# Kernel optimization log

Measured on AMD Instinct MI355X. Metric: run time of the kernel, lower is better.

## Reference

```python
import jax, jax.numpy as jnp
import numpy as np

B, H = 1, 512
NVAR, NCLS = 16384, 65536
NP, NM = 4096, 4096
NEG = -1e30


def setup_inputs() -> dict:
    key = jax.random.key(0)
    ks = jax.random.split(key, 16)
    s = 0.02  # weight init scale
    return {
        "literal_emb": jax.random.normal(ks[0], (B, 2 * NVAR, H), jnp.float32),
        "clause_emb": jax.random.normal(ks[1], (B, NCLS, H), jnp.float32),
        "pos_idx": jax.random.randint(ks[2], (NP,), 0, NCLS),
        "neg_idx": jax.random.randint(ks[3], (NM,), 0, NCLS),
        "keep_mask": jax.random.randint(ks[4], (NP, NM), 0, 2).astype(bool),
        "taken_mask": jax.random.uniform(ks[5], (NP, NM)) < 0.01,  # sparse exclusion set
        "var_K_w": s * jax.random.normal(ks[6], (H, H), jnp.float32),
        "var_K_b": jnp.zeros((H,), jnp.float32),
        "var_Q_w": s * jax.random.normal(ks[7], (H, H), jnp.float32),
        "var_Q_b": jnp.zeros((H,), jnp.float32),
        "var_attn_w": s * jax.random.normal(ks[8], (1, H), jnp.float32),
        "var_attn_b": jnp.zeros((1,), jnp.float32),
        "W_Q_w": s * jax.random.normal(ks[9], (H, H), jnp.float32),
        "W_Q_b": jnp.zeros((H,), jnp.float32),
        "W_K_w": s * jax.random.normal(ks[10], (H, H), jnp.float32),
        "W_K_b": jnp.zeros((H,), jnp.float32),
    }


def reference(literal_emb, clause_emb, pos_idx, neg_idx, keep_mask, taken_mask,
              var_K_w, var_K_b, var_Q_w, var_Q_b, var_attn_w, var_attn_b,
              W_Q_w, W_Q_b, W_K_w, W_K_b):
    n_vars = literal_emb.shape[1] // 2
    # --- select_var: additive attention over positive literals ---
    K = literal_emb[:, :n_vars]                       # [B, V, H]
    K_t = K @ var_K_w.T + var_K_b                     # [B, V, H]
    Q = clause_emb.sum(axis=1)                        # [B, H] (C_aggr='sum')
    Q_t = Q @ var_Q_w.T + var_Q_b                     # [B, H]
    u = (jnp.tanh(K_t + Q_t[:, None, :]) @ var_attn_w.T + var_attn_b)[..., 0]  # [B, V]
    log_score = jax.nn.log_softmax(u, axis=-1)
    var_logp = jnp.max(log_score, axis=-1)            # [B]
    var_idx = jnp.argmax(log_score, axis=-1)          # [B]
    # --- clause-pair attention over pivot pos/neg clause pools ---
    q = clause_emb[:, pos_idx] @ W_Q_w.T + W_Q_b      # [B, NP, H]
    k = clause_emb[:, neg_idx] @ W_K_w.T + W_K_b      # [B, NM, H]
    h = q.shape[-1]
    scores = jnp.einsum('bnh,bmh->bnm', q, k) / jnp.sqrt(jnp.float32(h))
    # mask_grid_asym: drop invalid (keep_mask==0) and already-taken pairs, log-normalize
    valid = keep_mask & (~taken_mask)                 # [NP, NM]
    masked = jnp.where(valid[None], scores, jnp.float32(NEG))
    flat = masked.reshape(masked.shape[0], -1)        # [B, NP*NM]
    logp = jax.nn.log_softmax(flat, axis=-1)
    C_logp = jnp.max(logp, axis=-1)                   # [B]
    C_flat = jnp.argmax(logp, axis=-1)                # [B]
    M = scores.shape[-1]
    ci, cj = C_flat // M, C_flat % M
    c_idx_pos = pos_idx[ci]                           # map back to global clause ids
    c_idx_neg = neg_idx[cj]
    c_logp = C_logp + var_logp                        # [B]
    return (c_logp, c_idx_pos, c_idx_neg, var_idx)
```

## Files before the change

### kernel.cpp

```cpp
#include <hip/hip_runtime.h>
#include <hip/hip_bf16.h>
#include <math.h>

#define HH 512
#define NVARS 16384
#define NPOS 4096
#define NMS 4096
#define NEGV -1.0e30f
#define RSQRT_H 0.04419417382415922f

typedef unsigned short u16;
typedef __attribute__((ext_vector_type(8))) short bf16x8;
typedef __attribute__((ext_vector_type(4))) float f32x4;

struct SPart { float m; float s; int a; int pad; };

__device__ inline u16 f2bf(float f) {
  unsigned u = __float_as_uint(f);
  unsigned r = (u + 0x7fffu + ((u >> 16) & 1u)) >> 16;
  return (u16)r;
}
__device__ inline float bf2f(u16 h) { return __uint_as_float(((unsigned)h) << 16); }

__device__ inline void wreduce_maxidx(float& v, int& idx) {
#pragma unroll
  for (int m = 1; m < 64; m <<= 1) {
    float ov = __shfl_xor(v, m, 64);
    int oi = __shfl_xor(idx, m, 64);
    if (ov > v || (ov == v && oi < idx)) { v = ov; idx = oi; }
  }
}

__device__ inline float wreduce_sum(float v) {
#pragma unroll
  for (int m = 1; m < 64; m <<= 1) v += __shfl_xor(v, m, 64);
  return v;
}

__device__ __forceinline__ void stage_frag(const u16* src, u16* dst) {
  __builtin_amdgcn_global_load_lds(
      (const __attribute__((address_space(1))) void*)src,
      (__attribute__((address_space(3))) void*)dst, 16, 0, 0);
}

__device__ __forceinline__ void do_tofrag(
    const float* __restrict__ src, u16* __restrict__ hi, u16* __restrict__ lo,
    int frag, int lane) {
  const int R = frag >> 4, K = frag & 15;
  const float* p = src + (size_t)(R * 16 + (lane & 15)) * HH + K * 32 + (lane >> 4) * 8;
  float v[8];
  *(float4*)&v[0] = *(const float4*)p;
  *(float4*)&v[4] = *(const float4*)(p + 4);
  u16 h[8], l[8];
#pragma unroll
  for (int e = 0; e < 8; ++e) { h[e] = f2bf(v[e]); l[e] = f2bf(v[e] - bf2f(h[e])); }
  size_t base = (size_t)frag * 512 + (size_t)lane * 8;
  *(ushort4*)(hi + base) = *(ushort4*)&h[0];
  *(ushort4*)(hi + base + 4) = *(ushort4*)&h[4];
  *(ushort4*)(lo + base) = *(ushort4*)&l[0];
  *(ushort4*)(lo + base + 4) = *(ushort4*)&l[4];
}

__global__ __launch_bounds__(256) void wtofrag_kernel(
    const float* __restrict__ varKw, u16* __restrict__ wkhi, u16* __restrict__ wklo,
    const float* __restrict__ WQw, u16* __restrict__ pwqhi, u16* __restrict__ pwqlo,
    const float* __restrict__ WKw, u16* __restrict__ pwkhi, u16* __restrict__ pwklo) {
  const int wb = blockIdx.x;
  const int m = wb >> 7;
  const int frag = (wb & 127) * 4 + (threadIdx.x >> 6);
  const float* src = (m == 0) ? varKw : (m == 1) ? WQw : WKw;
  u16* hi = (m == 0) ? wkhi : (m == 1) ? pwqhi : pwkhi;
  u16* lo = (m == 0) ? wklo : (m == 1) ? pwqlo : pwklo;
  do_tofrag(src, hi, lo, frag, threadIdx.x & 63);
}

__global__ __launch_bounds__(256) void stream_kernel(
    const float* __restrict__ clause, double* __restrict__ qpart,
    const float* __restrict__ lit, u16* __restrict__ lithi, u16* __restrict__ litlo,
    const void* __restrict__ keep, const void* __restrict__ taken,
    unsigned long long* __restrict__ vmask) {
  const int bid = blockIdx.x;
  const int t = threadIdx.x;
  if (bid < 2048) {
    const int fg = t & 127;
    const int rh = t >> 7;
    const float* base = clause + ((size_t)bid * 32 + rh * 16) * HH + fg * 4;
    float4 v[16];
#pragma unroll
    for (int u = 0; u < 16; ++u)
      v[u] = *(const float4*)(base + (size_t)u * HH);
    double a0 = 0.0, a1 = 0.0, a2 = 0.0, a3 = 0.0;
#pragma unroll
    for (int u = 0; u < 16; ++u) {
      a0 += (double)v[u].x; a1 += (double)v[u].y;
      a2 += (double)v[u].z; a3 += (double)v[u].w;
    }
    double* o = qpart + (size_t)(bid * 2 + rh) * HH + fg * 4;
    o[0] = a0; o[1] = a1; o[2] = a2; o[3] = a3;
  } else if (bid < 6144) {
    const int frag = (bid - 2048) * 4 + (t >> 6);
    do_tofrag(lit, lithi, litlo, frag, t & 63);
  } else {
    __shared__ unsigned half_[256];
    const int pb = bid - 6144;
    const unsigned* kw = (const unsigned*)keep;
    int f = 1;
#pragma unroll
    for (int i = 0; i < 16; ++i) f &= (kw[i] <= 1u);
    const size_t e = (size_t)pb * 8192 + (size_t)t * 32;
    unsigned b = 0;
    if (f) {
      const unsigned* kp = (const unsigned*)keep + e;
      const unsigned* tp = (const unsigned*)taken + e;
      uint4 kv[8], tv[8];
#pragma unroll
      for (int c = 0; c < 8; ++c) { kv[c] = *(const uint4*)(kp + c * 4); }
#pragma unroll
      for (int c = 0; c < 8; ++c) { tv[c] = *(const uint4*)(tp + c * 4); }
#pragma unroll
      for (int c = 0; c < 8; ++c) {
        b |= (unsigned)(kv[c].x && !tv[c].x) << (c * 4 + 0);
        b |= (unsigned)(kv[c].y && !tv[c].y) << (c * 4 + 1);
        b |= (unsigned)(kv[c].z && !tv[c].z) << (c * 4 + 2);
        b |= (unsigned)(kv[c].w && !tv[c].w) << (c * 4 + 3);
      }
    } else {
      const unsigned char* kp = (const unsigned char*)keep + e;
      const unsigned char* tp = (const unsigned char*)taken + e;
      uint4 k0 = *(const uint4*)kp, k1 = *(const uint4*)(kp + 16);
      uint4 t0 = *(const uint4*)tp, t1 = *(const uint4*)(tp + 16);
      unsigned kws[8] = {k0.x, k0.y, k0.z, k0.w, k1.x, k1.y, k1.z, k1.w};
      unsigned tws[8] = {t0.x, t0.y, t0.z, t0.w, t1.x, t1.y, t1.z, t1.w};
#pragma unroll
      for (int c = 0; c < 8; ++c)
#pragma unroll
        for (int y = 0; y < 4; ++y) {
          unsigned kb = (kws[c] >> (8 * y)) & 0xffu;
          unsigned tb = (tws[c] >> (8 * y)) & 0xffu;
          b |= (unsigned)(kb && !tb) << (c * 4 + y);
        }
    }
    half_[t] = b;
    __syncthreads();
    if (t < 128) {
      unsigned long long m = (unsigned long long)half_[t * 2] |
                             ((unsigned long long)half_[t * 2 + 1] << 32);
      vmask[(size_t)pb * 128 + t] = m;
    }
  }
}

__global__ __launch_bounds__(256) void qred_kernel(
    const double* __restrict__ qpart, double* __restrict__ Qd) {
  __shared__ double red[256];
  const int t = threadIdx.x;
  const int h = blockIdx.x * 16 + (t & 15);
  const int chunk = t >> 4;
  double s = 0.0;
  for (int j0 = 0; j0 < 256; j0 += 8) {
    double v[8];
#pragma unroll
    for (int u = 0; u < 8; ++u)
      v[u] = qpart[(size_t)(chunk * 256 + j0 + u) * HH + h];
#pragma unroll
    for (int u = 0; u < 8; ++u) s += v[u];
  }
  red[t] = s;
  __syncthreads();
  for (int off = 8; off > 0; off >>= 1) {
    if (chunk < off) red[t] += red[t + off * 16];
    __syncthreads();
  }
  if (t < 16) Qd[blockIdx.x * 16 + t] = red[t];
}

__global__ __launch_bounds__(256) void prepmv_kernel(
    const double* __restrict__ Qd, const float* __restrict__ varQw,
    const float* __restrict__ varQb, const float* __restrict__ varKb,
    float* __restrict__ tvec) {
  __shared__ double red[256];
  const int t = threadIdx.x;
  const int h = blockIdx.x * 16 + (t & 15);
  const int chunk = t >> 4;
  const float* wrow = varQw + (size_t)h * HH + chunk * 32;
  const double* qd = Qd + chunk * 32;
  double s = 0.0;
  for (int j = 0; j < 32; ++j) s += qd[j] * (double)wrow[j];
  red[t] = s;
  __syncthreads();
  for (int off = 8; off > 0; off >>= 1) {
    if (chunk < off) red[t] += red[t + off * 16];
    __syncthreads();
  }
  if (t < 16) {
    int hh = blockIdx.x * 16 + t;
    tvec[hh] = (float)(red[t] + (double)varQb[hh] + (double)varKb[hh]);
  }
}

#define MFMA16(A, B)                                                                 \
  _Pragma("unroll") for (int i_ = 0; i_ < 4; ++i_)                                   \
  _Pragma("unroll") for (int j_ = 0; j_ < 4; ++j_)                                   \
    acc[i_][j_] = __builtin_amdgcn_mfma_f32_16x16x32_bf16(A[i_], B[j_], acc[i_][j_], 0, 0, 0);

#define MFMAS(AH, AL, BH, BL)                                                        \
  do { MFMA16(AH, BH) MFMA16(AH, BL) MFMA16(AL, BH) } while (0)

__global__ __launch_bounds__(256, 3) void proj_kernel(
    const float* __restrict__ clause,
    const int* __restrict__ pos_idx, const int* __restrict__ neg_idx,
    const u16* __restrict__ pwqhi, const u16* __restrict__ pwqlo,
    const u16* __restrict__ pwkhi, const u16* __restrict__ pwklo,
    const float* __restrict__ bQ, const float* __restrict__ bK,
    u16* __restrict__ qhi, u16* __restrict__ qlo,
    u16* __restrict__ khi, u16* __restrict__ klo) {
  const int* __restrict__ idx = blockIdx.z ? neg_idx : pos_idx;
  const u16* __restrict__ whp = blockIdx.z ? pwkhi : pwqhi;
  const u16* __restrict__ wlp = blockIdx.z ? pwklo : pwqlo;
  const float* __restrict__ bias = blockIdx.z ? bK : bQ;
  u16* __restrict__ ohi = blockIdx.z ? khi : qhi;
  u16* __restrict__ olo = blockIdx.z ? klo : qlo;

  const int t = threadIdx.x, lane = t & 63, wid = t >> 6;
  const int wn = wid & 1, wm = wid >> 1;
  const int row0 = blockIdx.x * 128;
  const int col0 = blockIdx.y * 128;

  const float* bptr[4];
#pragma unroll
  for (int j = 0; j < 4; ++j) {
    int g = idx[row0 + wn * 64 + j * 16 + (lane & 15)];
    bptr[j] = clause + (size_t)g * HH + (lane >> 4) * 8;
  }
  const size_t abase = (size_t)((col0 >> 4) + wm * 4) * 8192 + (size_t)lane * 8;

  f32x4 acc[4][4] = {};
#pragma unroll
  for (int s = 0; s < 16; ++s) {
    float rB[4][8];
    bf16x8 aH[4], aL[4], bH[4], bL[4];
#pragma unroll
    for (int f = 0; f < 4; ++f) {
      *(float4*)&rB[f][0] = *(const float4*)(bptr[f] + s * 32);
      *(float4*)&rB[f][4] = *(const float4*)(bptr[f] + s * 32 + 4);
      size_t oa = abase + (size_t)f * 8192 + (size_t)s * 512;
      aH[f] = *(const bf16x8*)(whp + oa);
      aL[f] = *(const bf16x8*)(wlp + oa);
    }
#pragma unroll
    for (int f = 0; f < 4; ++f)
#pragma unroll
      for (int e = 0; e < 8; ++e) {
        float v = rB[f][e];
        u16 h = f2bf(v);
        bH[f][e] = (short)h;
        bL[f][e] = (short)f2bf(v - bf2f(h));
      }
    MFMA16(aH, bH)
    MFMA16(aL, bH)
    MFMA16(aH, bL)
  }

  const int q4 = lane >> 4;
#pragma unroll
  for (int i = 0; i < 4; ++i) {
    const int hbase = col0 + wm * 64 + i * 16 + q4 * 4;
    float b0 = bias[hbase + 0], b1 = bias[hbase + 1];
    float b2 = bias[hbase + 2], b3 = bias[hbase + 3];
    const int lane16 = (lane & 15) + ((i & 1) * 2 + (q4 >> 1)) * 16;
    const int sub = (q4 & 1) * 4;
#pragma unroll
    for (int j = 0; j < 4; ++j) {
      const int frag = ((row0 + wn * 64 + j * 16) >> 4) * 16 +
                       ((col0 + wm * 64 + i * 16) >> 5);
      size_t base = (size_t)frag * 512 + (size_t)lane16 * 8 + sub;
      ushort4 hv, lv;
      float v;
      v = acc[i][j][0] + b0; hv.x = f2bf(v); lv.x = f2bf(v - bf2f(hv.x));
      v = acc[i][j][1] + b1; hv.y = f2bf(v); lv.y = f2bf(v - bf2f(hv.y));
      v = acc[i][j][2] + b2; hv.z = f2bf(v); lv.z = f2bf(v - bf2f(hv.z));
      v = acc[i][j][3] + b3; hv.w = f2bf(v); lv.w = f2bf(v - bf2f(hv.w));
      *(ushort4*)(ohi + base) = hv;
      *(ushort4*)(olo + base) = lv;
    }
  }
}

__global__ __launch_bounds__(256, 2) void ktu_kernel(
    const u16* __restrict__ lithi, const u16* __restrict__ litlo,
    const u16* __restrict__ wkhi, const u16* __restrict__ wklo,
    const float* __restrict__ tvec, const float* __restrict__ attnw,
    float* __restrict__ upart) {
  __shared__ __align__(16) u16 lds[2][4][8][512];
  const int t = threadIdx.x, lane = t & 63, wid = t >> 6;
  const int wn = wid & 1, wm = wid >> 1;
  const int row0 = blockIdx.x * 128;
  const int l8 = lane * 8;

  const u16* sa = (wid == 0) ? lithi : (wid == 1) ? litlo : (wid == 2) ? wkhi : wklo;
  const int rb = (wid < 2) ? (row0 >> 4) : (blockIdx.y * 8);
  const u16* sab = sa + (size_t)rb * 8192 + l8;

#define KSTAGE(buf, s)                                                        \
  _Pragma("unroll") for (int f_ = 0; f_ < 8; ++f_)                            \
    stage_frag(sab + (size_t)f_ * 8192 + (size_t)(s) * 512,                   \
               &lds[buf][wid][f_][0]);

  KSTAGE(0, 0)
  f32x4 acc[4][4] = {};
#pragma unroll
  for (int s = 0; s < 16; ++s) {
    __syncthreads();
    if (s < 15) { KSTAGE((s + 1) & 1, s + 1) }
    const int b = s & 1;
    bf16x8 aH[4], aL[4], bH[4], bL[4];
#pragma unroll
    for (int f = 0; f < 4; ++f) {
      aH[f] = *(const bf16x8*)&lds[b][0][wn * 4 + f][l8];
      aL[f] = *(const bf16x8*)&lds[b][1][wn * 4 + f][l8];
      bH[f] = *(const bf16x8*)&lds[b][2][wm * 4 + f][l8];
      bL[f] = *(const bf16x8*)&lds[b][3][wm * 4 + f][l8];
    }
    MFMAS(aH, aL, bH, bL);
  }
#undef KSTAGE

  const int cbase = blockIdx.y * 128 + wm * 64;
  float tv[4], aw[4];
#pragma unroll
  for (int j = 0; j < 4; ++j) {
    int c = cbase + j * 16 + (lane & 15);
    tv[j] = tvec[c]; aw[j] = attnw[c];
  }
  float us[4][4];
#pragma unroll
  for (int i = 0; i < 4; ++i)
#pragma unroll
    for (int r = 0; r < 4; ++r) {
      float s = 0.f;
#pragma unroll
      for (int j = 0; j < 4; ++j) {
        float x = acc[i][j][r] + tv[j];
        float th = 1.0f - 2.0f / (__expf(2.0f * x) + 1.0f);
        s += th * aw[j];
      }
      us[i][r] = s;
    }
#pragma unroll
  for (int m = 1; m < 16; m <<= 1)
#pragma unroll
    for (int i = 0; i < 4; ++i)
#pragma unroll
      for (int r = 0; r < 4; ++r) us[i][r] += __shfl_xor(us[i][r], m, 64);
  if ((lane & 15) == 0) {
#pragma unroll
    for (int i = 0; i < 4; ++i)
#pragma unroll
      for (int r = 0; r < 4; ++r) {
        int row = row0 + wn * 64 + i * 16 + (lane >> 4) * 4 + r;
        upart[(size_t)(blockIdx.y * 2 + wm) * NVARS + row] = us[i][r];
      }
  }
}

__global__ __launch_bounds__(256, 2) void scores_kernel(
    const u16* __restrict__ qhi, const u16* __restrict__ qlo,
    const u16* __restrict__ khi, const u16* __restrict__ klo,
    const unsigned long long* __restrict__ vmask, SPart* __restrict__ parts) {
  __shared__ __align__(16) u16 lds[2][4][8][512];
  __shared__ unsigned long long mrow[128][2];
  __shared__ float s_rv[4]; __shared__ int s_ri[4]; __shared__ float s_rs[4];
  __shared__ float s_bm; __shared__ int s_ba;

  const int t = threadIdx.x;
  const int lane = t & 63;
  const int wid = t >> 6;
  const int wn = wid & 1, wm = wid >> 1;
  const int l8 = lane * 8;

  const int bid = blockIdx.x;
  const int xcd = bid & 7, p = bid >> 3;
  const int sp = p >> 6, q = p & 63;
  const int g = xcd * 2 + sp;
  const int bx = (g & 3) * 8 + (q & 7);
  const int by = (g >> 2) * 8 + (q >> 3);

  const int n0 = by * 128;
  const int m0 = bx * 128;

  const u16* sa = (wid == 0) ? qhi : (wid == 1) ? qlo : (wid == 2) ? khi : klo;
  const int rb = (wid < 2) ? (n0 >> 4) : (m0 >> 4);
  const u16* sab = sa + (size_t)rb * 8192 + l8;

#define SSTAGE(buf, s)                                                        \
  _Pragma("unroll") for (int f_ = 0; f_ < 8; ++f_)                            \
    stage_frag(sab + (size_t)f_ * 8192 + (size_t)(s) * 512,                   \
               &lds[buf][wid][f_][0]);

  {
    int r = t >> 1, w = t & 1;
    mrow[r][w] = vmask[(size_t)(n0 + r) * (NMS / 64) + (m0 >> 6) + w];
  }

  SSTAGE(0, 0)
  f32x4 acc[4][4] = {};
#pragma unroll
  for (int s = 0; s < 16; ++s) {
    __syncthreads();
    if (s < 15) { SSTAGE((s + 1) & 1, s + 1) }
    const int b = s & 1;
    bf16x8 aH[4], aL[4], bH[4], bL[4];
#pragma unroll
    for (int f = 0; f < 4; ++f) {
      aH[f] = *(const bf16x8*)&lds[b][0][wn * 4 + f][l8];
      aL[f] = *(const bf16x8*)&lds[b][1][wn * 4 + f][l8];
      bH[f] = *(const bf16x8*)&lds[b][2][wm * 4 + f][l8];
      bL[f] = *(const bf16x8*)&lds[b][3][wm * 4 + f][l8];
    }
    MFMAS(aH, aL, bH, bL);
  }
#undef SSTAGE

  const int rbase = wn * 64 + (lane >> 4) * 4;
  const int cb15 = (lane & 15);

  float mv = NEGV; int mi = 0x7fffffff;
#pragma unroll
  for (int i = 0; i < 4; ++i) {
#pragma unroll
    for (int r = 0; r < 4; ++r) {
      int rl = rbase + i * 16 + r;
      unsigned long long ww = mrow[rl][wm];
      int gb = (n0 + rl) * NMS + m0;
#pragma unroll
      for (int j = 0; j < 4; ++j) {
        int bit = j * 16 + cb15;
        int cl = wm * 64 + bit;
        float sv = acc[i][j][r] * RSQRT_H;
        acc[i][j][r] = sv;
        bool valid = ((ww >> bit) & 1ull) != 0;
        if (valid && (sv > mv || (sv == mv && gb + cl < mi))) { mv = sv; mi = gb + cl; }
      }
    }
  }
  wreduce_maxidx(mv, mi);
  if ((t & 63) == 0) { s_rv[wid] = mv; s_ri[wid] = mi; }
  __syncthreads();
  if (t == 0) {
    float bm = s_rv[0]; int ba = s_ri[0];
    for (int w = 1; w < 4; ++w)
      if (s_rv[w] > bm || (s_rv[w] == bm && s_ri[w] < ba)) { bm = s_rv[w]; ba = s_ri[w]; }
    s_bm = bm; s_ba = ba;
  }
  __syncthreads();
  const float bm = s_bm;

  float se = 0.f;
#pragma unroll
  for (int i = 0; i < 4; ++i) {
#pragma unroll
    for (int r = 0; r < 4; ++r) {
      int rl = rbase + i * 16 + r;
      unsigned long long ww = mrow[rl][wm];
#pragma unroll
      for (int j = 0; j < 4; ++j) {
        int bit = j * 16 + cb15;
        bool valid = ((ww >> bit) & 1ull) != 0;
        if (valid) se += __expf(acc[i][j][r] - bm);
      }
    }
  }
  se = wreduce_sum(se);
  if ((t & 63) == 0) s_rs[wid] = se;
  __syncthreads();
  if (t == 0) {
    SPart pt;
    pt.m = s_bm;
    pt.s = s_rs[0] + s_rs[1] + s_rs[2] + s_rs[3];
    pt.a = s_ba; pt.pad = 0;
    parts[by * 32 + bx] = pt;
  }
}

__global__ __launch_bounds__(256) void usum_kernel(
    const float* __restrict__ upart, SPart* __restrict__ uparts2) {
  __shared__ float s_rv[4]; __shared__ int s_ri[4]; __shared__ float s_rs[4];
  __shared__ float s_bm; __shared__ int s_ba;
  const int t = threadIdx.x;
  const int i = blockIdx.x * 256 + t;
  float u = 0.f;
#pragma unroll
  for (int p = 0; p < 8; ++p) u += upart[(size_t)p * NVARS + i];
  float mv = u; int mi = i;
  wreduce_maxidx(mv, mi);
  if ((t & 63) == 0) { s_rv[t >> 6] = mv; s_ri[t >> 6] = mi; }
  __syncthreads();
  if (t == 0) {
    float bm = s_rv[0]; int ba = s_ri[0];
    for (int w = 1; w < 4; ++w)
      if (s_rv[w] > bm || (s_rv[w] == bm && s_ri[w] < ba)) { bm = s_rv[w]; ba = s_ri[w]; }
    s_bm = bm; s_ba = ba;
  }
  __syncthreads();
  float se = __expf(u - s_bm);
  se = wreduce_sum(se);
  if ((t & 63) == 0) s_rs[t >> 6] = se;
  __syncthreads();
  if (t == 0) {
    SPart p;
    p.m = s_bm;
    p.s = s_rs[0] + s_rs[1] + s_rs[2] + s_rs[3];
    p.a = s_ba; p.pad = 0;
    uparts2[blockIdx.x] = p;
  }
}

__global__ __launch_bounds__(256) void final_kernel(
    const SPart* __restrict__ uparts2, const SPart* __restrict__ parts,
    const int* __restrict__ pos_idx, const int* __restrict__ neg_idx,
    float* __restrict__ out) {
  __shared__ float s_rv[4]; __shared__ int s_ri[4]; __shared__ float s_rs[4];
  __shared__ float s_umax; __shared__ int s_uarg; __shared__ float s_usum;
  __shared__ float s_gm; __shared__ int s_ga;
  const int t = threadIdx.x;

  float mv = -3.0e38f; int mi = 0x7fffffff;
  SPart up;
  if (t < 64) {
    up = uparts2[t];
    mv = up.m; mi = up.a;
  }
  wreduce_maxidx(mv, mi);
  if ((t & 63) == 0) { s_rv[t >> 6] = mv; s_ri[t >> 6] = mi; }
  __syncthreads();
  if (t == 0) {
    float bm = s_rv[0]; int ba = s_ri[0];
    for (int w = 1; w < 4; ++w)
      if (s_rv[w] > bm || (s_rv[w] == bm && s_ri[w] < ba)) { bm = s_rv[w]; ba = s_ri[w]; }
    s_umax = bm; s_uarg = ba;
  }
  __syncthreads();
  float se = (t < 64) ? up.s * __expf(up.m - s_umax) : 0.f;
  se = wreduce_sum(se);
  if ((t & 63) == 0) s_rs[t >> 6] = se;
  __syncthreads();
  if (t == 0) s_usum = s_rs[0] + s_rs[1] + s_rs[2] + s_rs[3];
  __syncthreads();

  mv = NEGV; mi = 0x7fffffff;
  for (int i = t; i < 1024; i += 256) {
    SPart p = parts[i];
    if (p.m > mv || (p.m == mv && p.a < mi)) { mv = p.m; mi = p.a; }
  }
  wreduce_maxidx(mv, mi);
  if ((t & 63) == 0) { s_rv[t >> 6] = mv; s_ri[t >> 6] = mi; }
  __syncthreads();
  if (t == 0) {
    float bm = s_rv[0]; int ba = s_ri[0];
    for (int w = 1; w < 4; ++w)
      if (s_rv[w] > bm || (s_rv[w] == bm && s_ri[w] < ba)) { bm = s_rv[w]; ba = s_ri[w]; }
    s_gm = bm; s_ga = ba;
  }
  __syncthreads();
  const float gm = s_gm;
  float ss = 0.f;
  for (int i = t; i < 1024; i += 256) {
    SPart p = parts[i];
    ss += p.s * __expf(p.m - gm);
  }
  ss = wreduce_sum(ss);
  if ((t & 63) == 0) s_rs[t >> 6] = ss;
  __syncthreads();
  if (t == 0) {
    float gsum = s_rs[0] + s_rs[1] + s_rs[2] + s_rs[3];
    float c_logp = -logf(gsum) - logf(s_usum);
    int ga = s_ga;
    if (ga == 0x7fffffff) ga = 0;
    int ci = ga >> 12, cj = ga & 4095;
    out[0] = c_logp;
    out[1] = (float)pos_idx[ci];
    out[2] = (float)neg_idx[cj];
    out[3] = (float)s_uarg;
  }
}

extern "C" void kernel_launch(void* const* d_in, const int* in_sizes, int n_in,
                              void* d_out, int out_size, void* d_ws, size_t ws_size,
                              hipStream_t stream) {
  (void)in_sizes; (void)n_in; (void)out_size; (void)ws_size;
  const float* lit    = (const float*)d_in[0];
  const float* clause = (const float*)d_in[1];
  const int* pos_idx  = (const int*)d_in[2];
  const int* neg_idx  = (const int*)d_in[3];
  const void* keep    = d_in[4];
  const void* taken   = d_in[5];
  const float* varKw  = (const float*)d_in[6];
  const float* varKb  = (const float*)d_in[7];
  const float* varQw  = (const float*)d_in[8];
  const float* varQb  = (const float*)d_in[9];
  const float* attnw  = (const float*)d_in[10];
  const float* WQw    = (const float*)d_in[12];
  const float* WQb    = (const float*)d_in[13];
  const float* WKw    = (const float*)d_in[14];
  const float* WKb    = (const float*)d_in[15];

  char* ws = (char*)d_ws;
  size_t off = 0;
  auto alloc = [&](size_t b) {
    char* p = ws + off;
    off = (off + b + 255) & ~(size_t)255;
    return p;
  };
  double* qpart              = (double*)alloc((size_t)4096 * HH * 8);
  double* Qd                 = (double*)alloc(HH * 8);
  float* tvec                = (float*)alloc(HH * 4);
  float* upart               = (float*)alloc(8 * (size_t)NVARS * 4);
  unsigned long long* vmask  = (unsigned long long*)alloc((size_t)NPOS * (NMS / 64) * 8);
  u16* qhi                   = (u16*)alloc((size_t)NPOS * HH * 2);
  u16* qlo                   = (u16*)alloc((size_t)NPOS * HH * 2);
  u16* khi                   = (u16*)alloc((size_t)NMS * HH * 2);
  u16* klo                   = (u16*)alloc((size_t)NMS * HH * 2);
  u16* wkhi                  = (u16*)alloc((size_t)HH * HH * 2);
  u16* wklo                  = (u16*)alloc((size_t)HH * HH * 2);
  u16* pwqhi                 = (u16*)alloc((size_t)HH * HH * 2);
  u16* pwqlo                 = (u16*)alloc((size_t)HH * HH * 2);
  u16* pwkhi                 = (u16*)alloc((size_t)HH * HH * 2);
  u16* pwklo                 = (u16*)alloc((size_t)HH * HH * 2);
  u16* lithi                 = (u16*)alloc((size_t)NVARS * HH * 2);
  u16* litlo                 = (u16*)alloc((size_t)NVARS * HH * 2);
  SPart* parts               = (SPart*)alloc(1024 * sizeof(SPart));
  SPart* uparts2             = (SPart*)alloc(64 * sizeof(SPart));

  wtofrag_kernel<<<384, 256, 0, stream>>>(varKw, wkhi, wklo,
                                          WQw, pwqhi, pwqlo,
                                          WKw, pwkhi, pwklo);
  proj_kernel<<<dim3(32, 4, 2), 256, 0, stream>>>(clause, pos_idx, neg_idx,
                                                  pwqhi, pwqlo, pwkhi, pwklo,
                                                  WQb, WKb,
                                                  qhi, qlo, khi, klo);
  stream_kernel<<<8192, 256, 0, stream>>>(clause, qpart, lit, lithi, litlo,
                                          keep, taken, vmask);
  qred_kernel<<<32, 256, 0, stream>>>(qpart, Qd);
  prepmv_kernel<<<32, 256, 0, stream>>>(Qd, varQw, varQb, varKb, tvec);
  scores_kernel<<<1024, 256, 0, stream>>>(qhi, qlo, khi, klo, vmask, parts);
  ktu_kernel<<<dim3(128, 4), 256, 0, stream>>>(lithi, litlo, wkhi, wklo,
                                               tvec, attnw, upart);
  usum_kernel<<<64, 256, 0, stream>>>(upart, uparts2);
  final_kernel<<<1, 256, 0, stream>>>(uparts2, parts, pos_idx, neg_idx,
                                      (float*)d_out);
}
```

Measured before the change: 246.1 us.

## Fuse mask packing, clause sum and literal split into scores kernel

Merges the stream kernel and the scores kernel into one launch. The scores blocks now build their validity bitmask straight from keep/taken instead of going through a global vmask buffer. The other blocks of the same launch do the clause-sum partials and the literal hi/lo split. The scores GEMM also drops its double-buffered LDS staging and loads fragments straight from global memory into registers. This saves a launch and the vmask round trip and lets memory-bound work overlap MFMA work, at the cost of possibly worse load latency hiding and more register pressure.

```diff
diff --git a/kernel.cpp b/kernel.cpp
--- a/kernel.cpp
+++ b/kernel.cpp
@@ -10,6 +10,7 @@
 #define RSQRT_H 0.04419417382415922f
 
 typedef unsigned short u16;
+typedef unsigned char u8;
 typedef __attribute__((ext_vector_type(8))) short bf16x8;
 typedef __attribute__((ext_vector_type(4))) float f32x4;
 
@@ -60,6 +61,26 @@
   *(ushort4*)(lo + base) = *(ushort4*)&l[0];
   *(ushort4*)(lo + base + 4) = *(ushort4*)&l[4];
 }
+
+#define MFMA16(A, B)                                                                 \
+  _Pragma("unroll") for (int i_ = 0; i_ < 4; ++i_)                                   \
+  _Pragma("unroll") for (int j_ = 0; j_ < 4; ++j_)                                   \
+    acc[i_][j_] = __builtin_amdgcn_mfma_f32_16x16x32_bf16(A[i_], B[j_], acc[i_][j_], 0, 0, 0);
+
+#define MFMAS(AH, AL, BH, BL)                                                        \
+  do { MFMA16(AH, BH) MFMA16(AH, BL) MFMA16(AL, BH) } while (0)
+
+#define LOADF(s, AH, AL, BH, BL, PAH, PAL, PBH, PBL)                                 \
+  do {                                                                               \
+    _Pragma("unroll") for (int f_ = 0; f_ < 4; ++f_) {                               \
+      size_t oa_ = abase + (size_t)f_ * 8192 + (size_t)(s) * 512;                    \
+      size_t ob_ = bbase + (size_t)f_ * 8192 + (size_t)(s) * 512;                    \
+      AH[f_] = *(const bf16x8*)(PAH + oa_);                                          \
+      AL[f_] = *(const bf16x8*)(PAL + oa_);                                          \
+      BH[f_] = *(const bf16x8*)(PBH + ob_);                                          \
+      BL[f_] = *(const bf16x8*)(PBL + ob_);                                          \
+    }                                                                                \
+  } while (0)
 
 __global__ __launch_bounds__(256) void wtofrag_kernel(
     const float* __restrict__ varKw, u16* __restrict__ wkhi, u16* __restrict__ wklo,
@@ -73,138 +94,6 @@
   u16* lo = (m == 0) ? wklo : (m == 1) ? pwqlo : pwklo;
   do_tofrag(src, hi, lo, frag, threadIdx.x & 63);
 }
-
-__global__ __launch_bounds__(256) void stream_kernel(
-    const float* __restrict__ clause, double* __restrict__ qpart,
-    const float* __restrict__ lit, u16* __restrict__ lithi, u16* __restrict__ litlo,
-    const void* __restrict__ keep, const void* __restrict__ taken,
-    unsigned long long* __restrict__ vmask) {
-  const int bid = blockIdx.x;
-  const int t = threadIdx.x;
-  if (bid < 2048) {
-    const int fg = t & 127;
-    const int rh = t >> 7;
-    const float* base = clause + ((size_t)bid * 32 + rh * 16) * HH + fg * 4;
-    float4 v[16];
-#pragma unroll
-    for (int u = 0; u < 16; ++u)
-      v[u] = *(const float4*)(base + (size_t)u * HH);
-    double a0 = 0.0, a1 = 0.0, a2 = 0.0, a3 = 0.0;
-#pragma unroll
-    for (int u = 0; u < 16; ++u) {
-      a0 += (double)v[u].x; a1 += (double)v[u].y;
-      a2 += (double)v[u].z; a3 += (double)v[u].w;
-    }
-    double* o = qpart + (size_t)(bid * 2 + rh) * HH + fg * 4;
-    o[0] = a0; o[1] = a1; o[2] = a2; o[3] = a3;
-  } else if (bid < 6144) {
-    const int frag = (bid - 2048) * 4 + (t >> 6);
-    do_tofrag(lit, lithi, litlo, frag, t & 63);
-  } else {
-    __shared__ unsigned half_[256];
-    const int pb = bid - 6144;
-    const unsigned* kw = (const unsigned*)keep;
-    int f = 1;
-#pragma unroll
-    for (int i = 0; i < 16; ++i) f &= (kw[i] <= 1u);
-    const size_t e = (size_t)pb * 8192 + (size_t)t * 32;
-    unsigned b = 0;
-    if (f) {
-      const unsigned* kp = (const unsigned*)keep + e;
-      const unsigned* tp = (const unsigned*)taken + e;
-      uint4 kv[8], tv[8];
-#pragma unroll
-      for (int c = 0; c < 8; ++c) { kv[c] = *(const uint4*)(kp + c * 4); }
-#pragma unroll
-      for (int c = 0; c < 8; ++c) { tv[c] = *(const uint4*)(tp + c * 4); }
-#pragma unroll
-      for (int c = 0; c < 8; ++c) {
-        b |= (unsigned)(kv[c].x && !tv[c].x) << (c * 4 + 0);
-        b |= (unsigned)(kv[c].y && !tv[c].y) << (c * 4 + 1);
-        b |= (unsigned)(kv[c].z && !tv[c].z) << (c * 4 + 2);
-        b |= (unsigned)(kv[c].w && !tv[c].w) << (c * 4 + 3);
-      }
-    } else {
-      const unsigned char* kp = (const unsigned char*)keep + e;
-      const unsigned char* tp = (const unsigned char*)taken + e;
-      uint4 k0 = *(const uint4*)kp, k1 = *(const uint4*)(kp + 16);
-      uint4 t0 = *(const uint4*)tp, t1 = *(const uint4*)(tp + 16);
-      unsigned kws[8] = {k0.x, k0.y, k0.z, k0.w, k1.x, k1.y, k1.z, k1.w};
-      unsigned tws[8] = {t0.x, t0.y, t0.z, t0.w, t1.x, t1.y, t1.z, t1.w};
-#pragma unroll
-      for (int c = 0; c < 8; ++c)
-#pragma unroll
-        for (int y = 0; y < 4; ++y) {
-          unsigned kb = (kws[c] >> (8 * y)) & 0xffu;
-          unsigned tb = (tws[c] >> (8 * y)) & 0xffu;
-          b |= (unsigned)(kb && !tb) << (c * 4 + y);
-        }
-    }
-    half_[t] = b;
-    __syncthreads();
-    if (t < 128) {
-      unsigned long long m = (unsigned long long)half_[t * 2] |
-                             ((unsigned long long)half_[t * 2 + 1] << 32);
-      vmask[(size_t)pb * 128 + t] = m;
-    }
-  }
-}
-
-__global__ __launch_bounds__(256) void qred_kernel(
-    const double* __restrict__ qpart, double* __restrict__ Qd) {
-  __shared__ double red[256];
-  const int t = threadIdx.x;
-  const int h = blockIdx.x * 16 + (t & 15);
-  const int chunk = t >> 4;
-  double s = 0.0;
-  for (int j0 = 0; j0 < 256; j0 += 8) {
-    double v[8];
-#pragma unroll
-    for (int u = 0; u < 8; ++u)
-      v[u] = qpart[(size_t)(chunk * 256 + j0 + u) * HH + h];
-#pragma unroll
-    for (int u = 0; u < 8; ++u) s += v[u];
-  }
-  red[t] = s;
-  __syncthreads();
-  for (int off = 8; off > 0; off >>= 1) {
-    if (chunk < off) red[t] += red[t + off * 16];
-    __syncthreads();
-  }
-  if (t < 16) Qd[blockIdx.x * 16 + t] = red[t];
-}
-
-__global__ __launch_bounds__(256) void prepmv_kernel(
-    const double* __restrict__ Qd, const float* __restrict__ varQw,
-    const float* __restrict__ varQb, const float* __restrict__ varKb,
-    float* __restrict__ tvec) {
-  __shared__ double red[256];
-  const int t = threadIdx.x;
-  const int h = blockIdx.x * 16 + (t & 15);
-  const int chunk = t >> 4;
-  const float* wrow = varQw + (size_t)h * HH + chunk * 32;
-  const double* qd = Qd + chunk * 32;
-  double s = 0.0;
-  for (int j = 0; j < 32; ++j) s += qd[j] * (double)wrow[j];
-  red[t] = s;
-  __syncthreads();
-  for (int off = 8; off > 0; off >>= 1) {
-    if (chunk < off) red[t] += red[t + off * 16];
-    __syncthreads();
-  }
-  if (t < 16) {
-    int hh = blockIdx.x * 16 + t;
-    tvec[hh] = (float)(red[t] + (double)varQb[hh] + (double)varKb[hh]);
-  }
-}
-
-#define MFMA16(A, B)                                                                 \
-  _Pragma("unroll") for (int i_ = 0; i_ < 4; ++i_)                                   \
-  _Pragma("unroll") for (int j_ = 0; j_ < 4; ++j_)                                   \
-    acc[i_][j_] = __builtin_amdgcn_mfma_f32_16x16x32_bf16(A[i_], B[j_], acc[i_][j_], 0, 0, 0);
-
-#define MFMAS(AH, AL, BH, BL)                                                        \
-  do { MFMA16(AH, BH) MFMA16(AH, BL) MFMA16(AL, BH) } while (0)
 
 __global__ __launch_bounds__(256, 3) void proj_kernel(
     const float* __restrict__ clause,
@@ -286,6 +175,221 @@
   }
 }
 
+__global__ __launch_bounds__(256, 3) void mega_kernel(
+    const u16* __restrict__ qhi, const u16* __restrict__ qlo,
+    const u16* __restrict__ khi, const u16* __restrict__ klo,
+    const void* __restrict__ keep, const void* __restrict__ taken,
+    SPart* __restrict__ parts,
+    const float* __restrict__ clause, double* __restrict__ qpart,
+    const float* __restrict__ lit, u16* __restrict__ lithi, u16* __restrict__ litlo) {
+  __shared__ unsigned long long mrow[128][2];
+  __shared__ float s_rv[4]; __shared__ int s_ri[4]; __shared__ float s_rs[4];
+  __shared__ float s_bm; __shared__ int s_ba;
+
+  const int id = blockIdx.x;
+  const int t = threadIdx.x;
+  const int lane = t & 63;
+  const int wid = t >> 6;
+
+  if (id >= 3072) {
+    const int frag = (id - 3072) * 4 + wid;
+    do_tofrag(lit, lithi, litlo, frag, lane);
+    return;
+  }
+  if (id >= 1024) {
+    const int qb = id - 1024;
+    const int fg = t & 127;
+    const int rh = t >> 7;
+    const float* base = clause + ((size_t)qb * 32 + rh * 16) * HH + fg * 4;
+    float4 v[16];
+#pragma unroll
+    for (int u = 0; u < 16; ++u)
+      v[u] = *(const float4*)(base + (size_t)u * HH);
+    double a0 = 0.0, a1 = 0.0, a2 = 0.0, a3 = 0.0;
+#pragma unroll
+    for (int u = 0; u < 16; ++u) {
+      a0 += (double)v[u].x; a1 += (double)v[u].y;
+      a2 += (double)v[u].z; a3 += (double)v[u].w;
+    }
+    double* o = qpart + (size_t)(qb * 2 + rh) * HH + fg * 4;
+    o[0] = a0; o[1] = a1; o[2] = a2; o[3] = a3;
+    return;
+  }
+
+  const int wn = wid & 1, wm = wid >> 1;
+
+  const int bid = id;
+  const int xcd = bid & 7, p = bid >> 3;
+  const int sp = p >> 6, q = p & 63;
+  const int g = xcd * 2 + sp;
+  const int bx = (g & 3) * 8 + (q & 7);
+  const int by = (g >> 2) * 8 + (q >> 3);
+
+  const int n0 = by * 128;
+  const int m0 = bx * 128;
+
+  {
+    const int r = t >> 1, half = t & 1;
+    const unsigned* kw = (const unsigned*)keep;
+    int f = 1;
+#pragma unroll
+    for (int i = 0; i < 16; ++i) f &= (kw[i] <= 1u);
+    unsigned long long w = 0;
+    if (!f) {
+      const u8* kp = (const u8*)keep + (size_t)(n0 + r) * NMS + m0 + half * 64;
+      const u8* tp = (const u8*)taken + (size_t)(n0 + r) * NMS + m0 + half * 64;
+#pragma unroll
+      for (int c = 0; c < 4; ++c) {
+        uint4 kv = *(const uint4*)(kp + c * 16);
+        uint4 tv = *(const uint4*)(tp + c * 16);
+        unsigned kws[4] = {kv.x, kv.y, kv.z, kv.w};
+        unsigned tws[4] = {tv.x, tv.y, tv.z, tv.w};
+#pragma unroll
+        for (int wi = 0; wi < 4; ++wi)
+#pragma unroll
+          for (int y = 0; y < 4; ++y) {
+            unsigned kb = (kws[wi] >> (8 * y)) & 0xffu;
+            unsigned tb = (tws[wi] >> (8 * y)) & 0xffu;
+            w |= (unsigned long long)(kb && !tb) << (c * 16 + wi * 4 + y);
+          }
+      }
+    } else {
+      const unsigned* kp = (const unsigned*)keep + (size_t)(n0 + r) * NMS + m0 + half * 64;
+      const unsigned* tp = (const unsigned*)taken + (size_t)(n0 + r) * NMS + m0 + half * 64;
+#pragma unroll
+      for (int c = 0; c < 16; ++c) {
+        uint4 kv = *(const uint4*)(kp + c * 4);
+        uint4 tv = *(const uint4*)(tp + c * 4);
+        w |= (unsigned long long)(kv.x && !tv.x) << (c * 4 + 0);
+        w |= (unsigned long long)(kv.y && !tv.y) << (c * 4 + 1);
+        w |= (unsigned long long)(kv.z && !tv.z) << (c * 4 + 2);
+        w |= (unsigned long long)(kv.w && !tv.w) << (c * 4 + 3);
+      }
+    }
+    mrow[r][half] = w;
+  }
+
+  const size_t abase = (size_t)((n0 >> 4) + wn * 4) * 8192 + (size_t)lane * 8;
+  const size_t bbase = (size_t)((m0 >> 4) + wm * 4) * 8192 + (size_t)lane * 8;
+
+  f32x4 acc[4][4] = {};
+#pragma unroll
+  for (int s = 0; s < 16; ++s) {
+    bf16x8 aH[4], aL[4], bH[4], bL[4];
+    LOADF(s, aH, aL, bH, bL, qhi, qlo, khi, klo);
+    MFMAS(aH, aL, bH, bL);
+  }
+  __syncthreads();
+
+  const int rbase = wn * 64 + (lane >> 4) * 4;
+  const int cb15 = (lane & 15);
+
+  float mv = NEGV; int mi = 0x7fffffff;
+#pragma unroll
+  for (int i = 0; i < 4; ++i) {
+#pragma unroll
+    for (int r = 0; r < 4; ++r) {
+      int rl = rbase + i * 16 + r;
+      unsigned long long ww = mrow[rl][wm];
+      int gb = (n0 + rl) * NMS + m0;
+#pragma unroll
+      for (int j = 0; j < 4; ++j) {
+        int bit = j * 16 + cb15;
+        int cl = wm * 64 + bit;
+        float sv = acc[i][j][r] * RSQRT_H;
+        acc[i][j][r] = sv;
+        bool valid = ((ww >> bit) & 1ull) != 0;
+        if (valid && (sv > mv || (sv == mv && gb + cl < mi))) { mv = sv; mi = gb + cl; }
+      }
+    }
+  }
+  wreduce_maxidx(mv, mi);
+  if ((t & 63) == 0) { s_rv[wid] = mv; s_ri[wid] = mi; }
+  __syncthreads();
+  if (t == 0) {
+    float bm = s_rv[0]; int ba = s_ri[0];
+    for (int w = 1; w < 4; ++w)
+      if (s_rv[w] > bm || (s_rv[w] == bm && s_ri[w] < ba)) { bm = s_rv[w]; ba = s_ri[w]; }
+    s_bm = bm; s_ba = ba;
+  }
+  __syncthreads();
+  const float bm = s_bm;
+
+  float se = 0.f;
+#pragma unroll
+  for (int i = 0; i < 4; ++i) {
+#pragma unroll
+    for (int r = 0; r < 4; ++r) {
+      int rl = rbase + i * 16 + r;
+      unsigned long long ww = mrow[rl][wm];
+#pragma unroll
+      for (int j = 0; j < 4; ++j) {
+        int bit = j * 16 + cb15;
+        bool valid = ((ww >> bit) & 1ull) != 0;
+        if (valid) se += __expf(acc[i][j][r] - bm);
+      }
+    }
+  }
+  se = wreduce_sum(se);
+  if ((t & 63) == 0) s_rs[wid] = se;
+  __syncthreads();
+  if (t == 0) {
+    SPart pt;
+    pt.m = s_bm;
+    pt.s = s_rs[0] + s_rs[1] + s_rs[2] + s_rs[3];
+    pt.a = s_ba; pt.pad = 0;
+    parts[by * 32 + bx] = pt;
+  }
+}
+
+__global__ __launch_bounds__(256) void qred_kernel(
+    const double* __restrict__ qpart, double* __restrict__ Qd) {
+  __shared__ double red[256];
+  const int t = threadIdx.x;
+  const int h = blockIdx.x * 16 + (t & 15);
+  const int chunk = t >> 4;
+  double s = 0.0;
+  for (int j0 = 0; j0 < 256; j0 += 8) {
+    double v[8];
+#pragma unroll
+    for (int u = 0; u < 8; ++u)
+      v[u] = qpart[(size_t)(chunk * 256 + j0 + u) * HH + h];
+#pragma unroll
+    for (int u = 0; u < 8; ++u) s += v[u];
+  }
+  red[t] = s;
+  __syncthreads();
+  for (int off = 8; off > 0; off >>= 1) {
+    if (chunk < off) red[t] += red[t + off * 16];
+    __syncthreads();
+  }
+  if (t < 16) Qd[blockIdx.x * 16 + t] = red[t];
+}
+
+__global__ __launch_bounds__(256) void prepmv_kernel(
+    const double* __restrict__ Qd, const float* __restrict__ varQw,
+    const float* __restrict__ varQb, const float* __restrict__ varKb,
+    float* __restrict__ tvec) {
+  __shared__ double red[256];
+  const int t = threadIdx.x;
+  const int h = blockIdx.x * 16 + (t & 15);
+  const int chunk = t >> 4;
+  const float* wrow = varQw + (size_t)h * HH + chunk * 32;
+  const double* qd = Qd + chunk * 32;
+  double s = 0.0;
+  for (int j = 0; j < 32; ++j) s += qd[j] * (double)wrow[j];
+  red[t] = s;
+  __syncthreads();
+  for (int off = 8; off > 0; off >>= 1) {
+    if (chunk < off) red[t] += red[t + off * 16];
+    __syncthreads();
+  }
+  if (t < 16) {
+    int hh = blockIdx.x * 16 + t;
+    tvec[hh] = (float)(red[t] + (double)varQb[hh] + (double)varKb[hh]);
+  }
+}
+
 __global__ __launch_bounds__(256, 2) void ktu_kernel(
     const u16* __restrict__ lithi, const u16* __restrict__ litlo,
     const u16* __restrict__ wkhi, const u16* __restrict__ wklo,
@@ -360,125 +464,6 @@
         int row = row0 + wn * 64 + i * 16 + (lane >> 4) * 4 + r;
         upart[(size_t)(blockIdx.y * 2 + wm) * NVARS + row] = us[i][r];
       }
-  }
-}
-
-__global__ __launch_bounds__(256, 2) void scores_kernel(
-    const u16* __restrict__ qhi, const u16* __restrict__ qlo,
-    const u16* __restrict__ khi, const u16* __restrict__ klo,
-    const unsigned long long* __restrict__ vmask, SPart* __restrict__ parts) {
-  __shared__ __align__(16) u16 lds[2][4][8][512];
-  __shared__ unsigned long long mrow[128][2];
-  __shared__ float s_rv[4]; __shared__ int s_ri[4]; __shared__ float s_rs[4];
-  __shared__ float s_bm; __shared__ int s_ba;
-
-  const int t = threadIdx.x;
-  const int lane = t & 63;
-  const int wid = t >> 6;
-  const int wn = wid & 1, wm = wid >> 1;
-  const int l8 = lane * 8;
-
-  const int bid = blockIdx.x;
-  const int xcd = bid & 7, p = bid >> 3;
-  const int sp = p >> 6, q = p & 63;
-  const int g = xcd * 2 + sp;
-  const int bx = (g & 3) * 8 + (q & 7);
-  const int by = (g >> 2) * 8 + (q >> 3);
-
-  const int n0 = by * 128;
-  const int m0 = bx * 128;
-
-  const u16* sa = (wid == 0) ? qhi : (wid == 1) ? qlo : (wid == 2) ? khi : klo;
-  const int rb = (wid < 2) ? (n0 >> 4) : (m0 >> 4);
-  const u16* sab = sa + (size_t)rb * 8192 + l8;
-
-#define SSTAGE(buf, s)                                                        \
-  _Pragma("unroll") for (int f_ = 0; f_ < 8; ++f_)                            \
-    stage_frag(sab + (size_t)f_ * 8192 + (size_t)(s) * 512,                   \
-               &lds[buf][wid][f_][0]);
-
-  {
-    int r = t >> 1, w = t & 1;
-    mrow[r][w] = vmask[(size_t)(n0 + r) * (NMS / 64) + (m0 >> 6) + w];
-  }
-
-  SSTAGE(0, 0)
-  f32x4 acc[4][4] = {};
-#pragma unroll
-  for (int s = 0; s < 16; ++s) {
-    __syncthreads();
-    if (s < 15) { SSTAGE((s + 1) & 1, s + 1) }
-    const int b = s & 1;
-    bf16x8 aH[4], aL[4], bH[4], bL[4];
-#pragma unroll
-    for (int f = 0; f < 4; ++f) {
-      aH[f] = *(const bf16x8*)&lds[b][0][wn * 4 + f][l8];
-      aL[f] = *(const bf16x8*)&lds[b][1][wn * 4 + f][l8];
-      bH[f] = *(const bf16x8*)&lds[b][2][wm * 4 + f][l8];
-      bL[f] = *(const bf16x8*)&lds[b][3][wm * 4 + f][l8];
-    }
-    MFMAS(aH, aL, bH, bL);
-  }
-#undef SSTAGE
-
-  const int rbase = wn * 64 + (lane >> 4) * 4;
-  const int cb15 = (lane & 15);
-
-  float mv = NEGV; int mi = 0x7fffffff;
-#pragma unroll
-  for (int i = 0; i < 4; ++i) {
-#pragma unroll
-    for (int r = 0; r < 4; ++r) {
-      int rl = rbase + i * 16 + r;
-      unsigned long long ww = mrow[rl][wm];
-      int gb = (n0 + rl) * NMS + m0;
-#pragma unroll
-      for (int j = 0; j < 4; ++j) {
-        int bit = j * 16 + cb15;
-        int cl = wm * 64 + bit;
-        float sv = acc[i][j][r] * RSQRT_H;
-        acc[i][j][r] = sv;
-        bool valid = ((ww >> bit) & 1ull) != 0;
-        if (valid && (sv > mv || (sv == mv && gb + cl < mi))) { mv = sv; mi = gb + cl; }
-      }
-    }
-  }
-  wreduce_maxidx(mv, mi);
-  if ((t & 63) == 0) { s_rv[wid] = mv; s_ri[wid] = mi; }
-  __syncthreads();
-  if (t == 0) {
-    float bm = s_rv[0]; int ba = s_ri[0];
-    for (int w = 1; w < 4; ++w)
-      if (s_rv[w] > bm || (s_rv[w] == bm && s_ri[w] < ba)) { bm = s_rv[w]; ba = s_ri[w]; }
-    s_bm = bm; s_ba = ba;
-  }
-  __syncthreads();
-  const float bm = s_bm;
-
-  float se = 0.f;
-#pragma unroll
-  for (int i = 0; i < 4; ++i) {
-#pragma unroll
-    for (int r = 0; r < 4; ++r) {
-      int rl = rbase + i * 16 + r;
-      unsigned long long ww = mrow[rl][wm];
-#pragma unroll
-      for (int j = 0; j < 4; ++j) {
-        int bit = j * 16 + cb15;
-        bool valid = ((ww >> bit) & 1ull) != 0;
-        if (valid) se += __expf(acc[i][j][r] - bm);
-      }
-    }
-  }
-  se = wreduce_sum(se);
-  if ((t & 63) == 0) s_rs[wid] = se;
-  __syncthreads();
-  if (t == 0) {
-    SPart pt;
-    pt.m = s_bm;
-    pt.s = s_rs[0] + s_rs[1] + s_rs[2] + s_rs[3];
-    pt.a = s_ba; pt.pad = 0;
-    parts[by * 32 + bx] = pt;
   }
 }
 
@@ -615,7 +600,6 @@
   double* Qd                 = (double*)alloc(HH * 8);
   float* tvec                = (float*)alloc(HH * 4);
   float* upart               = (float*)alloc(8 * (size_t)NVARS * 4);
-  unsigned long long* vmask  = (unsigned long long*)alloc((size_t)NPOS * (NMS / 64) * 8);
   u16* qhi                   = (u16*)alloc((size_t)NPOS * HH * 2);
   u16* qlo                   = (u16*)alloc((size_t)NPOS * HH * 2);
   u16* khi                   = (u16*)alloc((size_t)NMS * HH * 2);
@@ -638,11 +622,10 @@
                                                   pwqhi, pwqlo, pwkhi, pwklo,
                                                   WQb, WKb,
                                                   qhi, qlo, khi, klo);
-  stream_kernel<<<8192, 256, 0, stream>>>(clause, qpart, lit, lithi, litlo,
-                                          keep, taken, vmask);
+  mega_kernel<<<7168, 256, 0, stream>>>(qhi, qlo, khi, klo, keep, taken, parts,
+                                        clause, qpart, lit, lithi, litlo);
   qred_kernel<<<32, 256, 0, stream>>>(qpart, Qd);
   prepmv_kernel<<<32, 256, 0, stream>>>(Qd, varQw, varQb, varKb, tvec);
-  scores_kernel<<<1024, 256, 0, stream>>>(qhi, qlo, khi, klo, vmask, parts);
   ktu_kernel<<<dim3(128, 4), 256, 0, stream>>>(lithi, litlo, wkhi, wklo,
                                                tvec, attnw, upart);
   usum_kernel<<<64, 256, 0, stream>>>(upart, uparts2);
```

Result: slower. 258.2 us (+4.9%).
